# Performance work log

Hardware: AMD Instinct MI355X
Metric: run time of the kernel (lower is better)

The kernel has to match this reference:

```python
import jax, jax.numpy as jnp
import numpy as np

B, NP, PS, D = 4, 512, 16, 1024
NH = 4            # intra attention heads
HD = D // NH      # intra head dim
PH = 4            # pool heads
PHD = D // PH     # pool head dim
K = 5             # depthwise conv kernel size


def _rms_norm(x):
    # F.rms_norm with eps=None -> eps = finfo(dtype).eps, no learned weight
    eps = jnp.finfo(x.dtype).eps
    return x * jax.lax.rsqrt(jnp.mean(x * x, axis=-1, keepdims=True) + eps)


def setup_inputs() -> dict:
    key = jax.random.key(0)
    ks = jax.random.split(key, 12)
    s = 0.02
    return {
        "patch_byte_emb": jax.random.normal(ks[0], (B, NP, PS, D), jnp.float32),
        "local_pos": jax.random.normal(ks[1], (PS, D), jnp.float32) * 0.01,
        "w_gate": jax.random.normal(ks[2], (D, D), jnp.float32) * s,
        "w_in": jax.random.normal(ks[3], (D, D), jnp.float32) * s,
        "conv_w": jax.random.normal(ks[4], (D, 1, K), jnp.float32) * s,  # depthwise (out=D, in/groups=1, k)
        "w_qkv": jax.random.normal(ks[5], (3 * D, D), jnp.float32) * s,
        "w_intra_out": jax.random.normal(ks[6], (D, D), jnp.float32) * s,
        "w_pool": jax.random.normal(ks[7], (PH, D), jnp.float32) * s,
        "attn_temperature": jnp.ones((1,), jnp.float32),
        "w_up": jax.random.normal(ks[8], (D, D), jnp.float32) * s,
        "w_down": jax.random.normal(ks[9], (D, D), jnp.float32) * s,
        "w_out": jax.random.normal(ks[10], (D, D), jnp.float32) * s,
    }


def reference(patch_byte_emb, local_pos, w_gate, w_in, conv_w, w_qkv,
              w_intra_out, w_pool, attn_temperature, w_up, w_down, w_out):
    x = patch_byte_emb + local_pos[None, None]            # [B,NP,PS,D]
    x = _rms_norm(x)
    # SiLU-gated projection (CastedLinear: y = x @ W.T, no bias)
    x = jax.nn.silu(x @ w_gate.T) * (x @ w_in.T)
    bsz, num_patches, patch_size, model_dim = x.shape

    # depthwise causal-style conv1d: padding=4 both sides, then keep first PS outputs
    x_flat = x.reshape(bsz * num_patches, patch_size, model_dim).transpose(0, 2, 1)  # [BN,D,PS]
    conv_out = jax.lax.conv_general_dilated(
        x_flat, conv_w, window_strides=(1,), padding=[(K - 1, K - 1)],
        feature_group_count=model_dim,
        dimension_numbers=("NCH", "OIH", "NCH"))[:, :, :patch_size]
    x = x + conv_out.transpose(0, 2, 1).reshape(bsz, num_patches, patch_size, model_dim)

    # tiny per-patch self-attention
    x_sa = _rms_norm(x).reshape(bsz * num_patches, patch_size, model_dim)
    qkv = (x_sa @ w_qkv.T).reshape(bsz * num_patches, patch_size, 3, NH, HD)
    q, k, v = qkv[:, :, 0], qkv[:, :, 1], qkv[:, :, 2]    # [BN,PS,NH,HD]
    attn = jnp.einsum("bqhd,bkhd->bhqk", q, k) * (HD ** -0.5)
    attn = jax.nn.softmax(attn, axis=-1)
    sa = jnp.einsum("bhqk,bkhd->bqhd", attn, v).reshape(bsz * num_patches, patch_size, model_dim)
    x = x + (sa @ w_intra_out.T).reshape(bsz, num_patches, patch_size, model_dim)

    # multi-head attention pooling over patch positions
    x = _rms_norm(x)
    temp = jnp.clip(attn_temperature, 0.01, None).astype(x.dtype)  # [1]
    attn_logits = (x @ w_pool.T) / temp                   # [B,NP,PS,PH]
    attn_w = jax.nn.softmax(attn_logits.transpose(0, 1, 3, 2), axis=-1)  # [B,NP,PH,PS]
    x_heads = x.reshape(bsz, num_patches, patch_size, PH, PHD)
    pooled = jnp.einsum("bnhp,bnphd->bnhd", attn_w, x_heads).reshape(bsz, num_patches, model_dim)

    # post MLP + out proj
    y = pooled + (jax.nn.silu(_rms_norm(pooled) @ w_up.T) @ w_down.T)
    y = y @ w_out.T
    return _rms_norm(y)
```

## Files before the change

### kernel.cpp

```cpp
#include <hip/hip_runtime.h>
#include <cstdint>
#include <cstddef>


typedef __bf16 bf16x8 __attribute__((ext_vector_type(8)));
typedef float floatx4 __attribute__((ext_vector_type(4)));

#define DEV static __device__ __forceinline__

DEV unsigned short f2bf(float f) {
  union { float f; unsigned u; } x; x.f = f;
  unsigned r = x.u + 0x7fffu + ((x.u >> 16) & 1u);
  return (unsigned short)(r >> 16);
}
DEV float bf2f(unsigned short b) {
  union { unsigned u; float f; } x; x.u = ((unsigned)b) << 16;
  return x.f;
}
DEV float silu_f(float v) { return v / (1.f + __expf(-v)); }

DEV void gl_lds16(const unsigned short* g, unsigned short* l) {
  __builtin_amdgcn_global_load_lds(
      (const __attribute__((address_space(1))) void*)g,
      (__attribute__((address_space(3))) void*)l, 16, 0, 0);
}

DEV float block_reduce_sum(float v) {
  #pragma unroll
  for (int o = 32; o > 0; o >>= 1) v += __shfl_down(v, o, 64);
  __shared__ float s[4];
  int w = threadIdx.x >> 6;
  if ((threadIdx.x & 63) == 0) s[w] = v;
  __syncthreads();
  return s[0] + s[1] + s[2] + s[3];
}

struct CvtArgs {
  const float* src[7];
  unsigned short* dst[7];
  int blkoff[8];
};
__global__ __launch_bounds__(256) void cvt_all(CvtArgs a) {
  int b = blockIdx.x;
  int w = 0;
  #pragma unroll
  for (int i = 0; i < 6; i++) w += (b >= a.blkoff[i + 1]) ? 1 : 0;
  int i = (b - a.blkoff[w]) * 1024 + threadIdx.x * 4;
  float4 v = *(const float4*)(a.src[w] + i);
  ushort4 o;
  o.x = f2bf(v.x); o.y = f2bf(v.y); o.z = f2bf(v.z); o.w = f2bf(v.w);
  *(ushort4*)(a.dst[w] + i) = o;
}

__global__ __launch_bounds__(256) void prep_kernel(const float* __restrict__ pbe,
                                                   const float* __restrict__ pos,
                                                   unsigned short* __restrict__ xn) {
  int row = blockIdx.x;
  int t = row & 15;
  const float* ip = pbe + (size_t)row * 1024;
  const float* pp = pos + (size_t)t * 1024;
  int c = threadIdx.x * 4;
  float4 v = *(const float4*)(ip + c);
  float4 p = *(const float4*)(pp + c);
  v.x += p.x; v.y += p.y; v.z += p.z; v.w += p.w;
  float ss = v.x * v.x + v.y * v.y + v.z * v.z + v.w * v.w;
  ss = block_reduce_sum(ss);
  float sc = rsqrtf(ss * (1.f / 1024.f) + 1.1920929e-7f);
  ushort4 o;
  o.x = f2bf(v.x * sc); o.y = f2bf(v.y * sc); o.z = f2bf(v.z * sc); o.w = f2bf(v.w * sc);
  *(ushort4*)(xn + (size_t)row * 1024 + c) = o;
}

DEV float ldval(const float* p, size_t i) { return p[i]; }
DEV float ldval(const unsigned short* p, size_t i) { return bf2f(p[i]); }
DEV void stval(float* p, size_t i, float v) { p[i] = v; }
DEV void stval(unsigned short* p, size_t i, float v) { p[i] = f2bf(v); }

template <typename TI, typename TO>
__global__ __launch_bounds__(256) void rmsnorm_kernel(const TI* __restrict__ in,
                                                      TO* __restrict__ out) {
  size_t row = blockIdx.x;
  const TI* ip = in + row * 1024;
  TO* op = out + row * 1024;
  int c = threadIdx.x * 4;
  float v[4]; float ss = 0.f;
  #pragma unroll
  for (int j = 0; j < 4; j++) { v[j] = ldval(ip, c + j); ss += v[j] * v[j]; }
  ss = block_reduce_sum(ss);
  float sc = rsqrtf(ss * (1.f / 1024.f) + 1.1920929e-7f);
  #pragma unroll
  for (int j = 0; j < 4; j++) stval(op, c + j, v[j] * sc);
}


template <int R>
DEV void stage_rows(const unsigned short* __restrict__ src, int ldK,
                    unsigned short* lds, int k0, int pw, int lane) {
  constexpr int PER_WAVE = R / 32;
  #pragma unroll
  for (int d = 0; d < PER_WAVE; d++) {
    int di = pw * PER_WAVE + d;
    int r = di * 8 + (lane >> 3);
    int c = (lane & 7) ^ (r & 7);
    gl_lds16(src + (size_t)r * ldK + k0 + c * 8, lds + di * 512);
  }
}
DEV int frag_off64(int row, int g) {
  return row * 64 + ((g ^ (row & 7)) * 8);
}

template <int EPI, int TM, int TN>
__global__ __launch_bounds__(512) void gemm_ws(
    const unsigned short* __restrict__ A, const unsigned short* __restrict__ Bw,
    int M, int N, int K,
    float* __restrict__ outF, unsigned short* __restrict__ outB,
    const unsigned short* __restrict__ resB, const float* __restrict__ resF) {
  constexpr int AI = TM / 32;
  constexpr int BJ = TN / 32;
  __shared__ __align__(16) unsigned short As[2][TM * 64];
  __shared__ __align__(16) unsigned short Bs[2][TN * 64];
  const int tid = threadIdx.x;
  const int bm = blockIdx.y * TM, bn = blockIdx.x * TN;
  const int wave = tid >> 6, lane = tid & 63;
  const bool producer = wave >= 4;
  const int pw = wave & 3;
  const int wy = (wave & 3) >> 1, wx = wave & 1;
  const int l15 = lane & 15, quad = lane >> 4;

  const unsigned short* Ab = A + (size_t)bm * K;
  const unsigned short* Bb = Bw + (size_t)bn * K;

  floatx4 acc[AI][BJ];
  #pragma unroll
  for (int i = 0; i < AI; i++)
    #pragma unroll
    for (int j = 0; j < BJ; j++)
      #pragma unroll
      for (int r = 0; r < 4; r++) acc[i][j][r] = 0.f;

  int arow[AI], brow[BJ];
  #pragma unroll
  for (int i = 0; i < AI; i++) arow[i] = wy * (TM / 2) + i * 16 + l15;
  #pragma unroll
  for (int j = 0; j < BJ; j++) brow[j] = wx * (TN / 2) + j * 16 + l15;

  const int iters = K >> 6;
  if (producer) {
    stage_rows<TM>(Ab, K, As[0], 0, pw, lane);
    stage_rows<TN>(Bb, K, Bs[0], 0, pw, lane);
  }
  __syncthreads();
  for (int it = 0; it < iters; ++it) {
    const int cur = it & 1;
    if (producer) {
      if (it + 1 < iters) {
        stage_rows<TM>(Ab, K, As[cur ^ 1], (it + 1) << 6, pw, lane);
        stage_rows<TN>(Bb, K, Bs[cur ^ 1], (it + 1) << 6, pw, lane);
      }
    } else {
      #pragma unroll
      for (int h = 0; h < 2; h++) {
        bf16x8 afr[AI], bfr[BJ];
        #pragma unroll
        for (int i = 0; i < AI; i++)
          afr[i] = *(const bf16x8*)&As[cur][frag_off64(arow[i], h * 4 + quad)];
        #pragma unroll
        for (int j = 0; j < BJ; j++)
          bfr[j] = *(const bf16x8*)&Bs[cur][frag_off64(brow[j], h * 4 + quad)];
        #pragma unroll
        for (int i = 0; i < AI; i++)
          #pragma unroll
          for (int j = 0; j < BJ; j++)
            acc[i][j] = __builtin_amdgcn_mfma_f32_16x16x32_bf16(afr[i], bfr[j], acc[i][j], 0, 0, 0);
      }
    }
    __syncthreads();
  }

  if (producer) return;
  #pragma unroll
  for (int i = 0; i < AI; i++)
    #pragma unroll
    for (int j = 0; j < BJ; j++) {
      int gm = bm + wy * (TM / 2) + i * 16 + quad * 4;
      int gn = bn + wx * (TN / 2) + j * 16 + l15;
      #pragma unroll
      for (int r = 0; r < 4; r++) {
        float v = acc[i][j][r];
        size_t idx = (size_t)(gm + r) * N + gn;
        if (EPI == 0) outF[idx] = v;
        else if (EPI == 1) outB[idx] = f2bf(v);
        else if (EPI == 2) outB[idx] = f2bf(silu_f(v));
        else if (EPI == 3) outB[idx] = f2bf(v + bf2f(resB[idx]));
        else if (EPI == 4) outB[idx] = f2bf(v + resF[idx]);
      }
    }
}

__global__ __launch_bounds__(512) void gemm_dual_ws(
    const unsigned short* __restrict__ A, const unsigned short* __restrict__ Bg,
    const unsigned short* __restrict__ Bi, int M, int N, int K,
    unsigned short* __restrict__ outH) {
  __shared__ __align__(16) unsigned short As[2][128 * 64];
  __shared__ __align__(16) unsigned short Gs[2][64 * 64];
  __shared__ __align__(16) unsigned short Is[2][64 * 64];
  const int tid = threadIdx.x;
  const int bm = blockIdx.y * 128, bn = blockIdx.x * 64;
  const int wave = tid >> 6, lane = tid & 63;
  const bool producer = wave >= 4;
  const int pw = wave & 3;
  const int wy = (wave & 3) >> 1, wx = wave & 1;
  const int l15 = lane & 15, quad = lane >> 4;

  const unsigned short* Ab = A + (size_t)bm * K;
  const unsigned short* Gb = Bg + (size_t)bn * K;
  const unsigned short* Ib = Bi + (size_t)bn * K;

  floatx4 accg[4][2], acci[4][2];
  #pragma unroll
  for (int i = 0; i < 4; i++)
    #pragma unroll
    for (int j = 0; j < 2; j++)
      #pragma unroll
      for (int r = 0; r < 4; r++) { accg[i][j][r] = 0.f; acci[i][j][r] = 0.f; }

  int arow[4], brow[2];
  #pragma unroll
  for (int i = 0; i < 4; i++) arow[i] = wy * 64 + i * 16 + l15;
  #pragma unroll
  for (int j = 0; j < 2; j++) brow[j] = wx * 32 + j * 16 + l15;

  const int iters = K >> 6;
  if (producer) {
    stage_rows<128>(Ab, K, As[0], 0, pw, lane);
    stage_rows<64>(Gb, K, Gs[0], 0, pw, lane);
    stage_rows<64>(Ib, K, Is[0], 0, pw, lane);
  }
  __syncthreads();
  for (int it = 0; it < iters; ++it) {
    const int cur = it & 1;
    if (producer) {
      if (it + 1 < iters) {
        stage_rows<128>(Ab, K, As[cur ^ 1], (it + 1) << 6, pw, lane);
        stage_rows<64>(Gb, K, Gs[cur ^ 1], (it + 1) << 6, pw, lane);
        stage_rows<64>(Ib, K, Is[cur ^ 1], (it + 1) << 6, pw, lane);
      }
    } else {
      #pragma unroll
      for (int h = 0; h < 2; h++) {
        bf16x8 afr[4], gfr[2], ifr[2];
        #pragma unroll
        for (int i = 0; i < 4; i++)
          afr[i] = *(const bf16x8*)&As[cur][frag_off64(arow[i], h * 4 + quad)];
        #pragma unroll
        for (int j = 0; j < 2; j++) {
          gfr[j] = *(const bf16x8*)&Gs[cur][frag_off64(brow[j], h * 4 + quad)];
          ifr[j] = *(const bf16x8*)&Is[cur][frag_off64(brow[j], h * 4 + quad)];
        }
        #pragma unroll
        for (int i = 0; i < 4; i++)
          #pragma unroll
          for (int j = 0; j < 2; j++) {
            accg[i][j] = __builtin_amdgcn_mfma_f32_16x16x32_bf16(afr[i], gfr[j], accg[i][j], 0, 0, 0);
            acci[i][j] = __builtin_amdgcn_mfma_f32_16x16x32_bf16(afr[i], ifr[j], acci[i][j], 0, 0, 0);
          }
      }
    }
    __syncthreads();
  }

  if (producer) return;
  #pragma unroll
  for (int i = 0; i < 4; i++)
    #pragma unroll
    for (int j = 0; j < 2; j++) {
      int gm = bm + wy * 64 + i * 16 + quad * 4;
      int gn = bn + wx * 32 + j * 16 + l15;
      #pragma unroll
      for (int r = 0; r < 4; r++) {
        size_t idx = (size_t)(gm + r) * N + gn;
        outH[idx] = f2bf(silu_f(accg[i][j][r]) * acci[i][j][r]);
      }
    }
}

#define HS_LD 1040
__global__ __launch_bounds__(256) void conv_rms_kernel(const unsigned short* __restrict__ h,
                                                       const float* __restrict__ cw,
                                                       unsigned short* __restrict__ x2,
                                                       unsigned short* __restrict__ x2n) {
  int patch = blockIdx.x;
  __shared__ __align__(16) unsigned short hs[16 * HS_LD];
  __shared__ __align__(16) float cwp[5 * 1024];
  const int tid = threadIdx.x;
  size_t base = (size_t)patch * 16384;
  for (int idx = tid * 8; idx < 16384; idx += 256 * 8) {
    int row = idx >> 10, col = idx & 1023;
    *(uint4*)&hs[row * HS_LD + col] = *(const uint4*)&h[base + idx];
  }
  for (int i = tid; i < 5120; i += 256) {
    int c = i / 5, k = i - c * 5;
    cwp[k * 1024 + c] = cw[i];
  }
  __syncthreads();
  int t = tid >> 4;
  int lc = (tid & 15) * 8;
  float vals[8][8];
  float ss = 0.f;
  #pragma unroll
  for (int jb = 0; jb < 8; jb++) {
    int c = jb * 128 + lc;
    float tap[5][8];
    #pragma unroll
    for (int k = 0; k < 5; k++) {
      int tt = t + k - 4;
      if (tt >= 0) {
        uint4 v = *(const uint4*)&hs[tt * HS_LD + c];
        const unsigned short* vp = (const unsigned short*)&v;
        #pragma unroll
        for (int i = 0; i < 8; i++) tap[k][i] = bf2f(vp[i]);
      } else {
        #pragma unroll
        for (int i = 0; i < 8; i++) tap[k][i] = 0.f;
      }
    }
    float w[5][8];
    #pragma unroll
    for (int k = 0; k < 5; k++) {
      float4 a = *(const float4*)&cwp[k * 1024 + c];
      float4 b = *(const float4*)&cwp[k * 1024 + c + 4];
      w[k][0] = a.x; w[k][1] = a.y; w[k][2] = a.z; w[k][3] = a.w;
      w[k][4] = b.x; w[k][5] = b.y; w[k][6] = b.z; w[k][7] = b.w;
    }
    #pragma unroll
    for (int i = 0; i < 8; i++) {
      float acc = tap[4][i];
      #pragma unroll
      for (int k = 0; k < 5; k++) acc += w[k][i] * tap[k][i];
      vals[jb][i] = acc;
      ss += acc * acc;
    }
  }
  ss += __shfl_down(ss, 8, 16);
  ss += __shfl_down(ss, 4, 16);
  ss += __shfl_down(ss, 2, 16);
  ss += __shfl_down(ss, 1, 16);
  ss = __shfl(ss, 0, 16);
  float sc = rsqrtf(ss * (1.f / 1024.f) + 1.1920929e-7f);
  #pragma unroll
  for (int jb = 0; jb < 8; jb++) {
    ushort4 o2[2], on[2];
    #pragma unroll
    for (int i = 0; i < 8; i++) {
      ((unsigned short*)o2)[i] = f2bf(vals[jb][i]);
      ((unsigned short*)on)[i] = f2bf(vals[jb][i] * sc);
    }
    size_t off = base + (size_t)t * 1024 + jb * 128 + lc;
    *(uint4*)&x2[off] = *(uint4*)o2;
    *(uint4*)&x2n[off] = *(uint4*)on;
  }
}

__global__ __launch_bounds__(256) void attn_kernel(const unsigned short* __restrict__ qkv,
                                                   unsigned short* __restrict__ sa) {
  int patch = blockIdx.x;
  int head = blockIdx.y;
  const int tid = threadIdx.x;
  __shared__ float qs[16][260], ks[16][260], vs[16][260];
  __shared__ float sc[16][16];
  size_t base = (size_t)patch * 16 * 3072 + (size_t)head * 256;
  for (int idx = tid * 8; idx < 16 * 256; idx += 256 * 8) {
    int t = idx >> 8, d = idx & 255;
    size_t roff = base + (size_t)t * 3072 + d;
    uint4 qv = *(const uint4*)&qkv[roff];
    uint4 kv = *(const uint4*)&qkv[roff + 1024];
    uint4 vv = *(const uint4*)&qkv[roff + 2048];
    const unsigned short* qp = (const unsigned short*)&qv;
    const unsigned short* kp = (const unsigned short*)&kv;
    const unsigned short* vp = (const unsigned short*)&vv;
    #pragma unroll
    for (int i = 0; i < 8; i++) {
      qs[t][d + i] = bf2f(qp[i]);
      ks[t][d + i] = bf2f(kp[i]);
      vs[t][d + i] = bf2f(vp[i]);
    }
  }
  __syncthreads();
  {
    int t = tid >> 4, kk = tid & 15;
    float s = 0.f;
    for (int d = 0; d < 256; d += 4) {
      float4 q = *(const float4*)&qs[t][d];
      float4 k = *(const float4*)&ks[kk][d];
      s += q.x * k.x + q.y * k.y + q.z * k.z + q.w * k.w;
    }
    sc[t][kk] = s * 0.0625f;
  }
  __syncthreads();
  if (tid < 16) {
    float m = -1e30f;
    for (int kk = 0; kk < 16; kk++) m = fmaxf(m, sc[tid][kk]);
    float p[16], sum = 0.f;
    for (int kk = 0; kk < 16; kk++) { p[kk] = __expf(sc[tid][kk] - m); sum += p[kk]; }
    float inv = 1.f / sum;
    for (int kk = 0; kk < 16; kk++) sc[tid][kk] = p[kk] * inv;
  }
  __syncthreads();
  for (int idx = tid * 8; idx < 4096; idx += 256 * 8) {
    int t = idx >> 8, d = idx & 255;
    float o[8] = {0, 0, 0, 0, 0, 0, 0, 0};
    #pragma unroll
    for (int kk = 0; kk < 16; kk++) {
      float w = sc[t][kk];
      float4 v0 = *(const float4*)&vs[kk][d];
      float4 v1 = *(const float4*)&vs[kk][d + 4];
      o[0] += w * v0.x; o[1] += w * v0.y; o[2] += w * v0.z; o[3] += w * v0.w;
      o[4] += w * v1.x; o[5] += w * v1.y; o[6] += w * v1.z; o[7] += w * v1.w;
    }
    ushort4 ov[2];
    #pragma unroll
    for (int i = 0; i < 8; i++) ((unsigned short*)ov)[i] = f2bf(o[i]);
    *(uint4*)&sa[(size_t)(patch * 16 + t) * 1024 + head * 256 + d] = *(uint4*)ov;
  }
}

__global__ __launch_bounds__(256) void pool_kernel(const unsigned short* __restrict__ x3,
                                                   const float* __restrict__ wpool,
                                                   const float* __restrict__ tptr,
                                                   float* __restrict__ pooled,
                                                   unsigned short* __restrict__ pooledn) {
  int patch = blockIdx.x;
  __shared__ __align__(16) unsigned short xs[16 * 1024];
  __shared__ float lg[4][16], aw[4][16], srow[16];
  const int tid = threadIdx.x;
  size_t base = (size_t)patch * 16384;
  for (int idx = tid * 8; idx < 16384; idx += 256 * 8)
    *(uint4*)&xs[idx] = *(const uint4*)&x3[base + idx];
  __syncthreads();
  {
    int t = tid >> 4, sub = tid & 15;
    float ss = 0.f;
    for (int d = sub * 64; d < sub * 64 + 64; d += 4) {
      uint2 v = *(const uint2*)&xs[t * 1024 + d];
      const unsigned short* vp = (const unsigned short*)&v;
      #pragma unroll
      for (int i = 0; i < 4; i++) { float x = bf2f(vp[i]); ss += x * x; }
    }
    ss += __shfl_down(ss, 8, 16);
    ss += __shfl_down(ss, 4, 16);
    ss += __shfl_down(ss, 2, 16);
    ss += __shfl_down(ss, 1, 16);
    if (sub == 0) srow[t] = rsqrtf(ss * (1.f / 1024.f) + 1.1920929e-7f);
  }
  __syncthreads();
  {
    int pair = tid >> 2, sub = tid & 3;
    int t = pair >> 2, hh = pair & 3;
    float s = 0.f;
    for (int d = sub * 256; d < sub * 256 + 256; d++)
      s += bf2f(xs[t * 1024 + d]) * wpool[hh * 1024 + d];
    s += __shfl_down(s, 2, 64);
    s += __shfl_down(s, 1, 64);
    if (sub == 0) {
      float temp = fmaxf(tptr[0], 0.01f);
      lg[hh][t] = s * srow[t] / temp;
    }
  }
  __syncthreads();
  if (tid < 4) {
    int hh = tid;
    float m = -1e30f;
    for (int t = 0; t < 16; t++) m = fmaxf(m, lg[hh][t]);
    float p[16], sum = 0.f;
    for (int t = 0; t < 16; t++) { p[t] = __expf(lg[hh][t] - m); sum += p[t]; }
    float inv = 1.f / sum;
    for (int t = 0; t < 16; t++) aw[hh][t] = p[t] * inv;
  }
  __syncthreads();
  float ov[4]; int cs[4];
  float ss = 0.f;
  #pragma unroll
  for (int q = 0; q < 4; q++) {
    int c = tid + q * 256;
    int hh = c >> 8;
    float o = 0.f;
    #pragma unroll
    for (int t = 0; t < 16; t++) o += aw[hh][t] * srow[t] * bf2f(xs[t * 1024 + c]);
    ov[q] = o; cs[q] = c;
    ss += o * o;
  }
  ss = block_reduce_sum(ss);
  float scn = rsqrtf(ss * (1.f / 1024.f) + 1.1920929e-7f);
  #pragma unroll
  for (int q = 0; q < 4; q++) {
    pooled[(size_t)patch * 1024 + cs[q]] = ov[q];
    pooledn[(size_t)patch * 1024 + cs[q]] = f2bf(ov[q] * scn);
  }
}

extern "C" void kernel_launch(void* const* d_in, const int* in_sizes, int n_in,
                              void* d_out, int out_size, void* d_ws, size_t ws_size,
                              hipStream_t stream) {
  (void)in_sizes; (void)n_in; (void)out_size; (void)ws_size;
  const float* pbe  = (const float*)d_in[0];
  const float* lpos = (const float*)d_in[1];
  const float* wg   = (const float*)d_in[2];
  const float* wi   = (const float*)d_in[3];
  const float* cw   = (const float*)d_in[4];
  const float* wqkv = (const float*)d_in[5];
  const float* wio  = (const float*)d_in[6];
  const float* wpl  = (const float*)d_in[7];
  const float* temp = (const float*)d_in[8];
  const float* wup  = (const float*)d_in[9];
  const float* wdn  = (const float*)d_in[10];
  const float* wout = (const float*)d_in[11];
  float* outp = (float*)d_out;

  const int ROWS = 32768, Dm = 1024, NPAT = 2048;

  char* p = (char*)d_ws;
  auto take = [&](size_t nbytes) { void* r = (void*)p; p += (nbytes + 255) & ~(size_t)255; return r; };
  unsigned short* wg_b   = (unsigned short*)take((size_t)Dm * Dm * 2);
  unsigned short* wi_b   = (unsigned short*)take((size_t)Dm * Dm * 2);
  unsigned short* wqkv_b = (unsigned short*)take((size_t)3 * Dm * Dm * 2);
  unsigned short* wio_b  = (unsigned short*)take((size_t)Dm * Dm * 2);
  unsigned short* wup_b  = (unsigned short*)take((size_t)Dm * Dm * 2);
  unsigned short* wdn_b  = (unsigned short*)take((size_t)Dm * Dm * 2);
  unsigned short* wout_b = (unsigned short*)take((size_t)Dm * Dm * 2);
  unsigned short* slotA  = (unsigned short*)take((size_t)ROWS * Dm * 2);
  unsigned short* slotB  = (unsigned short*)take((size_t)ROWS * Dm * 2);
  unsigned short* slotC  = (unsigned short*)take((size_t)ROWS * Dm * 2);
  unsigned short* qkvB   = (unsigned short*)take((size_t)ROWS * 3 * Dm * 2);
  float*          pooled = (float*)take((size_t)NPAT * Dm * 4);
  unsigned short* pooledn= (unsigned short*)take((size_t)NPAT * Dm * 2);
  unsigned short* ubuf   = (unsigned short*)take((size_t)NPAT * Dm * 2);
  unsigned short* y1b    = (unsigned short*)take((size_t)NPAT * Dm * 2);
  float*          y2     = (float*)take((size_t)NPAT * Dm * 4);

  CvtArgs ca;
  ca.src[0] = wg;   ca.dst[0] = wg_b;
  ca.src[1] = wi;   ca.dst[1] = wi_b;
  ca.src[2] = wqkv; ca.dst[2] = wqkv_b;
  ca.src[3] = wio;  ca.dst[3] = wio_b;
  ca.src[4] = wup;  ca.dst[4] = wup_b;
  ca.src[5] = wdn;  ca.dst[5] = wdn_b;
  ca.src[6] = wout; ca.dst[6] = wout_b;
  int off = 0;
  for (int i = 0; i < 7; i++) { ca.blkoff[i] = off; off += (i == 2) ? 3072 : 1024; }
  ca.blkoff[7] = off;
  cvt_all<<<dim3(off), dim3(256), 0, stream>>>(ca);

  prep_kernel<<<dim3(ROWS), dim3(256), 0, stream>>>(pbe, lpos, slotA);
  gemm_dual_ws<<<dim3(Dm / 64, ROWS / 128), dim3(512), 0, stream>>>(
      slotA, wg_b, wi_b, ROWS, Dm, Dm, slotB);
  conv_rms_kernel<<<dim3(NPAT), dim3(256), 0, stream>>>(slotB, cw, slotC, slotA);
  gemm_ws<1, 128, 128><<<dim3(3 * Dm / 128, ROWS / 128), dim3(512), 0, stream>>>(
      slotA, wqkv_b, ROWS, 3 * Dm, Dm, nullptr, qkvB, nullptr, nullptr);
  attn_kernel<<<dim3(NPAT, 4), dim3(256), 0, stream>>>(qkvB, slotB);
  gemm_ws<3, 128, 128><<<dim3(Dm / 128, ROWS / 128), dim3(512), 0, stream>>>(
      slotB, wio_b, ROWS, Dm, Dm, nullptr, slotC, slotC, nullptr);
  pool_kernel<<<dim3(NPAT), dim3(256), 0, stream>>>(slotC, wpl, temp, pooled, pooledn);
  gemm_ws<2, 64, 128><<<dim3(Dm / 128, NPAT / 64), dim3(512), 0, stream>>>(
      pooledn, wup_b, NPAT, Dm, Dm, nullptr, ubuf, nullptr, nullptr);
  gemm_ws<4, 64, 128><<<dim3(Dm / 128, NPAT / 64), dim3(512), 0, stream>>>(
      ubuf, wdn_b, NPAT, Dm, Dm, nullptr, y1b, nullptr, pooled);
  gemm_ws<0, 64, 128><<<dim3(Dm / 128, NPAT / 64), dim3(512), 0, stream>>>(
      y1b, wout_b, NPAT, Dm, Dm, y2, nullptr, nullptr, nullptr);
  rmsnorm_kernel<float, float><<<dim3(NPAT), dim3(256), 0, stream>>>(y2, outp);
}
```

Measured before the change: 1.074 ms.

## Triple-buffer warp-specialized GEMM pipelines with explicit vmcnt waits and raw barriers

```diff
diff --git a/kernel.cpp b/kernel.cpp
--- a/kernel.cpp
+++ b/kernel.cpp
@@ -23,6 +23,14 @@
   __builtin_amdgcn_global_load_lds(
       (const __attribute__((address_space(1))) void*)g,
       (__attribute__((address_space(3))) void*)l, 16, 0, 0);
+}
+
+DEV void raw_barrier() { asm volatile("s_barrier" ::: "memory"); }
+template <int N> DEV void waitcnt_vm() {
+  if constexpr (N == 0) asm volatile("s_waitcnt vmcnt(0)" ::: "memory");
+  else if constexpr (N == 6) asm volatile("s_waitcnt vmcnt(6)" ::: "memory");
+  else if constexpr (N == 8) asm volatile("s_waitcnt vmcnt(8)" ::: "memory");
+  else static_assert(N == 0 || N == 6 || N == 8, "add literal");
 }
 
 DEV float block_reduce_sum(float v) {
@@ -110,15 +118,16 @@
 }
 
 template <int EPI, int TM, int TN>
-__global__ __launch_bounds__(512) void gemm_ws(
+__global__ __launch_bounds__(512) void gemm_ws3(
     const unsigned short* __restrict__ A, const unsigned short* __restrict__ Bw,
     int M, int N, int K,
     float* __restrict__ outF, unsigned short* __restrict__ outB,
     const unsigned short* __restrict__ resB, const float* __restrict__ resF) {
   constexpr int AI = TM / 32;
   constexpr int BJ = TN / 32;
-  __shared__ __align__(16) unsigned short As[2][TM * 64];
-  __shared__ __align__(16) unsigned short Bs[2][TN * 64];
+  constexpr int NDMA = (TM + TN) / 8 / 4;
+  __shared__ __align__(16) unsigned short As[3][TM * 64];
+  __shared__ __align__(16) unsigned short Bs[3][TN * 64];
   const int tid = threadIdx.x;
   const int bm = blockIdx.y * TM, bn = blockIdx.x * TN;
   const int wave = tid >> 6, lane = tid & 63;
@@ -148,14 +157,20 @@
   if (producer) {
     stage_rows<TM>(Ab, K, As[0], 0, pw, lane);
     stage_rows<TN>(Bb, K, Bs[0], 0, pw, lane);
-  }
-  __syncthreads();
+    stage_rows<TM>(Ab, K, As[1], 64, pw, lane);
+    stage_rows<TN>(Bb, K, Bs[1], 64, pw, lane);
+    waitcnt_vm<NDMA>();
+  }
+  raw_barrier();
+  int cur = 0, nx2 = 2;
   for (int it = 0; it < iters; ++it) {
-    const int cur = it & 1;
     if (producer) {
-      if (it + 1 < iters) {
-        stage_rows<TM>(Ab, K, As[cur ^ 1], (it + 1) << 6, pw, lane);
-        stage_rows<TN>(Bb, K, Bs[cur ^ 1], (it + 1) << 6, pw, lane);
+      if (it + 2 < iters) {
+        stage_rows<TM>(Ab, K, As[nx2], (it + 2) << 6, pw, lane);
+        stage_rows<TN>(Bb, K, Bs[nx2], (it + 2) << 6, pw, lane);
+        waitcnt_vm<NDMA>();
+      } else {
+        waitcnt_vm<0>();
       }
     } else {
       #pragma unroll
@@ -174,7 +189,9 @@
             acc[i][j] = __builtin_amdgcn_mfma_f32_16x16x32_bf16(afr[i], bfr[j], acc[i][j], 0, 0, 0);
       }
     }
-    __syncthreads();
+    raw_barrier();
+    cur = (cur == 2) ? 0 : cur + 1;
+    nx2 = (nx2 == 2) ? 0 : nx2 + 1;
   }
 
   if (producer) return;
@@ -197,13 +214,13 @@
     }
 }
 
-__global__ __launch_bounds__(512) void gemm_dual_ws(
+__global__ __launch_bounds__(512) void gemm_dual_ws3(
     const unsigned short* __restrict__ A, const unsigned short* __restrict__ Bg,
     const unsigned short* __restrict__ Bi, int M, int N, int K,
     unsigned short* __restrict__ outH) {
-  __shared__ __align__(16) unsigned short As[2][128 * 64];
-  __shared__ __align__(16) unsigned short Gs[2][64 * 64];
-  __shared__ __align__(16) unsigned short Is[2][64 * 64];
+  __shared__ __align__(16) unsigned short As[3][128 * 64];
+  __shared__ __align__(16) unsigned short Gs[3][64 * 64];
+  __shared__ __align__(16) unsigned short Is[3][64 * 64];
   const int tid = threadIdx.x;
   const int bm = blockIdx.y * 128, bn = blockIdx.x * 64;
   const int wave = tid >> 6, lane = tid & 63;
@@ -235,15 +252,22 @@
     stage_rows<128>(Ab, K, As[0], 0, pw, lane);
     stage_rows<64>(Gb, K, Gs[0], 0, pw, lane);
     stage_rows<64>(Ib, K, Is[0], 0, pw, lane);
-  }
-  __syncthreads();
+    stage_rows<128>(Ab, K, As[1], 64, pw, lane);
+    stage_rows<64>(Gb, K, Gs[1], 64, pw, lane);
+    stage_rows<64>(Ib, K, Is[1], 64, pw, lane);
+    waitcnt_vm<8>();
+  }
+  raw_barrier();
+  int cur = 0, nx2 = 2;
   for (int it = 0; it < iters; ++it) {
-    const int cur = it & 1;
     if (producer) {
-      if (it + 1 < iters) {
-        stage_rows<128>(Ab, K, As[cur ^ 1], (it + 1) << 6, pw, lane);
-        stage_rows<64>(Gb, K, Gs[cur ^ 1], (it + 1) << 6, pw, lane);
-        stage_rows<64>(Ib, K, Is[cur ^ 1], (it + 1) << 6, pw, lane);
+      if (it + 2 < iters) {
+        stage_rows<128>(Ab, K, As[nx2], (it + 2) << 6, pw, lane);
+        stage_rows<64>(Gb, K, Gs[nx2], (it + 2) << 6, pw, lane);
+        stage_rows<64>(Ib, K, Is[nx2], (it + 2) << 6, pw, lane);
+        waitcnt_vm<8>();
+      } else {
+        waitcnt_vm<0>();
       }
     } else {
       #pragma unroll
@@ -266,7 +290,9 @@
           }
       }
     }
-    __syncthreads();
+    raw_barrier();
+    cur = (cur == 2) ? 0 : cur + 1;
+    nx2 = (nx2 == 2) ? 0 : nx2 + 1;
   }
 
   if (producer) return;
@@ -551,20 +577,20 @@
   cvt_all<<<dim3(off), dim3(256), 0, stream>>>(ca);
 
   prep_kernel<<<dim3(ROWS), dim3(256), 0, stream>>>(pbe, lpos, slotA);
-  gemm_dual_ws<<<dim3(Dm / 64, ROWS / 128), dim3(512), 0, stream>>>(
+  gemm_dual_ws3<<<dim3(Dm / 64, ROWS / 128), dim3(512), 0, stream>>>(
       slotA, wg_b, wi_b, ROWS, Dm, Dm, slotB);
   conv_rms_kernel<<<dim3(NPAT), dim3(256), 0, stream>>>(slotB, cw, slotC, slotA);
-  gemm_ws<1, 128, 128><<<dim3(3 * Dm / 128, ROWS / 128), dim3(512), 0, stream>>>(
+  gemm_ws3<1, 128, 128><<<dim3(3 * Dm / 128, ROWS / 128), dim3(512), 0, stream>>>(
       slotA, wqkv_b, ROWS, 3 * Dm, Dm, nullptr, qkvB, nullptr, nullptr);
   attn_kernel<<<dim3(NPAT, 4), dim3(256), 0, stream>>>(qkvB, slotB);
-  gemm_ws<3, 128, 128><<<dim3(Dm / 128, ROWS / 128), dim3(512), 0, stream>>>(
+  gemm_ws3<3, 128, 128><<<dim3(Dm / 128, ROWS / 128), dim3(512), 0, stream>>>(
       slotB, wio_b, ROWS, Dm, Dm, nullptr, slotC, slotC, nullptr);
   pool_kernel<<<dim3(NPAT), dim3(256), 0, stream>>>(slotC, wpl, temp, pooled, pooledn);
-  gemm_ws<2, 64, 128><<<dim3(Dm / 128, NPAT / 64), dim3(512), 0, stream>>>(
+  gemm_ws3<2, 64, 128><<<dim3(Dm / 128, NPAT / 64), dim3(512), 0, stream>>>(
       pooledn, wup_b, NPAT, Dm, Dm, nullptr, ubuf, nullptr, nullptr);
-  gemm_ws<4, 64, 128><<<dim3(Dm / 128, NPAT / 64), dim3(512), 0, stream>>>(
+  gemm_ws3<4, 64, 128><<<dim3(Dm / 128, NPAT / 64), dim3(512), 0, stream>>>(
       ubuf, wdn_b, NPAT, Dm, Dm, nullptr, y1b, nullptr, pooled);
-  gemm_ws<0, 64, 128><<<dim3(Dm / 128, NPAT / 64), dim3(512), 0, stream>>>(
+  gemm_ws3<0, 64, 128><<<dim3(Dm / 128, NPAT / 64), dim3(512), 0, stream>>>(
       y1b, wout_b, NPAT, Dm, Dm, y2, nullptr, nullptr, nullptr);
   rmsnorm_kernel<float, float><<<dim3(NPAT), dim3(256), 0, stream>>>(y2, outp);
 }
```

After: 1.082 ms. About the same (+0.7%).

## Triple-buffer A tiles with depth-two prefetch and explicit vmcnt barriers in GEMMs

Applied to the files above, without the earlier changes.

```diff
diff --git a/kernel.cpp b/kernel.cpp
--- a/kernel.cpp
+++ b/kernel.cpp
@@ -23,6 +23,14 @@
   __builtin_amdgcn_global_load_lds(
       (const __attribute__((address_space(1))) void*)g,
       (__attribute__((address_space(3))) void*)l, 16, 0, 0);
+}
+
+DEV void raw_barrier() { asm volatile("s_barrier" ::: "memory"); }
+template <int N> DEV void waitcnt_vm() {
+  if constexpr (N == 0) asm volatile("s_waitcnt vmcnt(0)" ::: "memory");
+  else if constexpr (N == 2) asm volatile("s_waitcnt vmcnt(2)" ::: "memory");
+  else if constexpr (N == 4) asm volatile("s_waitcnt vmcnt(4)" ::: "memory");
+  else static_assert(N == 0 || N == 2 || N == 4, "add literal");
 }
 
 DEV float block_reduce_sum(float v) {
@@ -110,14 +118,14 @@
 }
 
 template <int EPI, int TM, int TN>
-__global__ __launch_bounds__(512) void gemm_ws(
+__global__ __launch_bounds__(512, 4) void gemm_ws(
     const unsigned short* __restrict__ A, const unsigned short* __restrict__ Bw,
     int M, int N, int K,
     float* __restrict__ outF, unsigned short* __restrict__ outB,
     const unsigned short* __restrict__ resB, const float* __restrict__ resF) {
   constexpr int AI = TM / 32;
   constexpr int BJ = TN / 32;
-  __shared__ __align__(16) unsigned short As[2][TM * 64];
+  __shared__ __align__(16) unsigned short As[3][TM * 64];
   __shared__ __align__(16) unsigned short Bs[2][TN * 64];
   const int tid = threadIdx.x;
   const int bm = blockIdx.y * TM, bn = blockIdx.x * TN;
@@ -146,27 +154,42 @@
 
   const int iters = K >> 6;
   if (producer) {
+    stage_rows<TN>(Bb, K, Bs[0], 0, pw, lane);
     stage_rows<TM>(Ab, K, As[0], 0, pw, lane);
-    stage_rows<TN>(Bb, K, Bs[0], 0, pw, lane);
-  }
-  __syncthreads();
+    if (iters > 1) {
+      stage_rows<TM>(Ab, K, As[1], 64, pw, lane);
+      waitcnt_vm<TM / 32>();
+    } else {
+      waitcnt_vm<0>();
+    }
+  }
+  raw_barrier();
+  int ac = 0;
   for (int it = 0; it < iters; ++it) {
-    const int cur = it & 1;
     if (producer) {
-      if (it + 1 < iters) {
-        stage_rows<TM>(Ab, K, As[cur ^ 1], (it + 1) << 6, pw, lane);
-        stage_rows<TN>(Bb, K, Bs[cur ^ 1], (it + 1) << 6, pw, lane);
+      const bool issueB = (it + 1 < iters);
+      const bool issueA = (it + 2 < iters);
+      if (issueB)
+        stage_rows<TN>(Bb, K, Bs[(it + 1) & 1], (it + 1) << 6, pw, lane);
+      if (issueA) {
+        int an = ac + 2; if (an >= 3) an -= 3;
+        stage_rows<TM>(Ab, K, As[an], (it + 2) << 6, pw, lane);
+        waitcnt_vm<TM / 32>();
+      } else {
+        waitcnt_vm<0>();
       }
     } else {
+      const unsigned short* Ac = As[ac];
+      const unsigned short* Bc = Bs[it & 1];
       #pragma unroll
       for (int h = 0; h < 2; h++) {
         bf16x8 afr[AI], bfr[BJ];
         #pragma unroll
         for (int i = 0; i < AI; i++)
-          afr[i] = *(const bf16x8*)&As[cur][frag_off64(arow[i], h * 4 + quad)];
+          afr[i] = *(const bf16x8*)&Ac[frag_off64(arow[i], h * 4 + quad)];
         #pragma unroll
         for (int j = 0; j < BJ; j++)
-          bfr[j] = *(const bf16x8*)&Bs[cur][frag_off64(brow[j], h * 4 + quad)];
+          bfr[j] = *(const bf16x8*)&Bc[frag_off64(brow[j], h * 4 + quad)];
         #pragma unroll
         for (int i = 0; i < AI; i++)
           #pragma unroll
@@ -174,7 +197,8 @@
             acc[i][j] = __builtin_amdgcn_mfma_f32_16x16x32_bf16(afr[i], bfr[j], acc[i][j], 0, 0, 0);
       }
     }
-    __syncthreads();
+    raw_barrier();
+    ac = (ac == 2) ? 0 : ac + 1;
   }
 
   if (producer) return;
@@ -197,11 +221,11 @@
     }
 }
 
-__global__ __launch_bounds__(512) void gemm_dual_ws(
+__global__ __launch_bounds__(512, 4) void gemm_dual_ws(
     const unsigned short* __restrict__ A, const unsigned short* __restrict__ Bg,
     const unsigned short* __restrict__ Bi, int M, int N, int K,
     unsigned short* __restrict__ outH) {
-  __shared__ __align__(16) unsigned short As[2][128 * 64];
+  __shared__ __align__(16) unsigned short As[3][128 * 64];
   __shared__ __align__(16) unsigned short Gs[2][64 * 64];
   __shared__ __align__(16) unsigned short Is[2][64 * 64];
   const int tid = threadIdx.x;
@@ -232,30 +256,47 @@
 
   const int iters = K >> 6;
   if (producer) {
-    stage_rows<128>(Ab, K, As[0], 0, pw, lane);
     stage_rows<64>(Gb, K, Gs[0], 0, pw, lane);
     stage_rows<64>(Ib, K, Is[0], 0, pw, lane);
-  }
-  __syncthreads();
+    stage_rows<128>(Ab, K, As[0], 0, pw, lane);
+    if (iters > 1) {
+      stage_rows<128>(Ab, K, As[1], 64, pw, lane);
+      waitcnt_vm<4>();
+    } else {
+      waitcnt_vm<0>();
+    }
+  }
+  raw_barrier();
+  int ac = 0;
   for (int it = 0; it < iters; ++it) {
-    const int cur = it & 1;
     if (producer) {
-      if (it + 1 < iters) {
-        stage_rows<128>(Ab, K, As[cur ^ 1], (it + 1) << 6, pw, lane);
-        stage_rows<64>(Gb, K, Gs[cur ^ 1], (it + 1) << 6, pw, lane);
-        stage_rows<64>(Ib, K, Is[cur ^ 1], (it + 1) << 6, pw, lane);
+      const bool issueB = (it + 1 < iters);
+      const bool issueA = (it + 2 < iters);
+      if (issueB) {
+        stage_rows<64>(Gb, K, Gs[(it + 1) & 1], (it + 1) << 6, pw, lane);
+        stage_rows<64>(Ib, K, Is[(it + 1) & 1], (it + 1) << 6, pw, lane);
+      }
+      if (issueA) {
+        int an = ac + 2; if (an >= 3) an -= 3;
+        stage_rows<128>(Ab, K, As[an], (it + 2) << 6, pw, lane);
+        waitcnt_vm<4>();
+      } else {
+        waitcnt_vm<0>();
       }
     } else {
+      const unsigned short* Ac = As[ac];
+      const unsigned short* Gc = Gs[it & 1];
+      const unsigned short* Ic = Is[it & 1];
       #pragma unroll
       for (int h = 0; h < 2; h++) {
         bf16x8 afr[4], gfr[2], ifr[2];
         #pragma unroll
         for (int i = 0; i < 4; i++)
-          afr[i] = *(const bf16x8*)&As[cur][frag_off64(arow[i], h * 4 + quad)];
+          afr[i] = *(const bf16x8*)&Ac[frag_off64(arow[i], h * 4 + quad)];
         #pragma unroll
         for (int j = 0; j < 2; j++) {
-          gfr[j] = *(const bf16x8*)&Gs[cur][frag_off64(brow[j], h * 4 + quad)];
-          ifr[j] = *(const bf16x8*)&Is[cur][frag_off64(brow[j], h * 4 + quad)];
+          gfr[j] = *(const bf16x8*)&Gc[frag_off64(brow[j], h * 4 + quad)];
+          ifr[j] = *(const bf16x8*)&Ic[frag_off64(brow[j], h * 4 + quad)];
         }
         #pragma unroll
         for (int i = 0; i < 4; i++)
@@ -266,7 +307,8 @@
           }
       }
     }
-    __syncthreads();
+    raw_barrier();
+    ac = (ac == 2) ? 0 : ac + 1;
   }
 
   if (producer) return;
```

Measured after the change: 1.030 ms. -4.1%, faster.
